# Optimization experiments

Measured on AMD Instinct MI355X. Metric: run time of the kernel, lower is better.

Reference implementation:

```python
import jax, jax.numpy as jnp
import numpy as np

B, T, C, H = 2, 2048, 1024, 16
D = C // H  # head dim = 64

def setup_inputs() -> dict:
    key = jax.random.key(0)
    k1, k2, k3 = jax.random.split(key, 3)
    x = jax.random.normal(k1, (B, T, C), dtype=jnp.float32)
    Wqkv = jax.random.normal(k2, (C, 3 * C), dtype=jnp.float32) * (1.0 / np.sqrt(C))
    bqkv = jnp.zeros((3 * C,), dtype=jnp.float32)
    Wo = jax.random.normal(k3, (C, C), dtype=jnp.float32) * (1.0 / np.sqrt(C))
    bo = jnp.zeros((C,), dtype=jnp.float32)
    return {"x": x, "Wqkv": Wqkv, "bqkv": bqkv, "Wo": Wo, "bo": bo}

def reference(x, Wqkv, bqkv, Wo, bo):
    b, t, c = x.shape
    qkv = x @ Wqkv + bqkv                              # [B,T,3C]
    q, k, v = jnp.split(qkv, 3, axis=-1)
    # [B,T,C] -> [B,H,T,D]
    q = q.reshape(b, t, H, D).transpose(0, 2, 1, 3)
    k = k.reshape(b, t, H, D).transpose(0, 2, 1, 3)
    v = v.reshape(b, t, H, D).transpose(0, 2, 1, 3)
    scores = jnp.einsum('bhqd,bhkd->bhqk', q, k) * (1.0 / np.sqrt(D))
    causal = jnp.tril(jnp.ones((t, t), dtype=bool))
    scores = jnp.where(causal, scores, -jnp.inf)
    probs = jax.nn.softmax(scores, axis=-1)           # dropout p=0 -> identity
    out = jnp.einsum('bhqk,bhkd->bhqd', probs, v)
    out = out.transpose(0, 2, 1, 3).reshape(b, t, c)
    return out @ Wo + bo
```

## Files before the change

kernel.cpp:

```cpp
#include <hip/hip_runtime.h>
#include <hip/hip_bf16.h>

typedef __attribute__((ext_vector_type(8))) short bf16x8;
typedef __attribute__((ext_vector_type(4))) short bf16x4;
typedef __attribute__((ext_vector_type(4))) float f32x4;

static __device__ __forceinline__ __hip_bfloat16 f2b(float f) {
    return __float2bfloat16(f);
}
static __device__ __forceinline__ unsigned pack2(float a, float b) {
    unsigned ua = (unsigned)__bfloat16_as_ushort(__float2bfloat16(a));
    unsigned ub = (unsigned)__bfloat16_as_ushort(__float2bfloat16(b));
    return ua | (ub << 16);
}
static __device__ __forceinline__ float exp2fast(float x) {
    return __builtin_amdgcn_exp2f(x);
}

#define QSCALE 0.1803368801111f

__global__ __launch_bounds__(256) void k_prep(
    const float* __restrict__ x, __hip_bfloat16* __restrict__ xb,
    const float* __restrict__ Wqkv, __hip_bfloat16* __restrict__ WqkvT,
    const float* __restrict__ Wo, __hip_bfloat16* __restrict__ WoT)
{
    const int bx = blockIdx.x;
    if (bx < 2048) {
        int i = bx * 256 + threadIdx.x;
        const int stride = 2048 * 256;
        for (; i < 1048576; i += stride) {
            float4 v = reinterpret_cast<const float4*>(x)[i];
            __hip_bfloat16* o = xb + 4 * (size_t)i;
            o[0] = f2b(v.x); o[1] = f2b(v.y); o[2] = f2b(v.z); o[3] = f2b(v.w);
        }
        return;
    }
    __shared__ float tile[32][33];
    const float* in;
    __hip_bfloat16* outp;
    int R, Cn, c0, r0;
    if (bx < 5120) {
        const int b = bx - 2048;
        in = Wqkv; outp = WqkvT; R = 1024; Cn = 3072;
        c0 = (b % 96) * 32; r0 = (b / 96) * 32;
    } else {
        const int b = bx - 5120;
        in = Wo; outp = WoT; R = 1024; Cn = 1024;
        c0 = (b & 31) * 32; r0 = (b >> 5) * 32;
    }
    const int tx = threadIdx.x & 31, ty = threadIdx.x >> 5;
#pragma unroll
    for (int i = 0; i < 32; i += 8)
        tile[ty + i][tx] = in[(size_t)(r0 + ty + i) * Cn + c0 + tx];
    __syncthreads();
#pragma unroll
    for (int i = 0; i < 32; i += 8)
        outp[(size_t)(c0 + ty + i) * R + r0 + tx] = f2b(tile[tx][ty + i]);
}

#define QK_STAGE(buf, kt)                                                       \
    {                                                                           \
        const int k0_ = (kt) << 5;                                              \
        _Pragma("unroll")                                                       \
        for (int i = 0; i < 2; ++i) {                                           \
            const int idx = i * 256 + tid;                                      \
            const int r_ = idx >> 2;                                            \
            const int j_ = idx & 3;                                             \
            const int js_ = j_ ^ ((r_ >> 1) & 3);                               \
            __builtin_amdgcn_global_load_lds(                                   \
                (const __attribute__((address_space(1))) void*)(A + (size_t)(m0 + r_) * K + k0_ + js_ * 8), \
                (__attribute__((address_space(3))) void*)(&As[buf][r_][j_ * 8]), 16, 0, 0); \
        }                                                                       \
        _Pragma("unroll")                                                       \
        for (int i = 0; i < 2; ++i) {                                           \
            const int idx = i * 256 + tid;                                      \
            const int r_ = idx >> 2;                                            \
            const int j_ = idx & 3;                                             \
            const int js_ = j_ ^ ((r_ >> 1) & 3);                               \
            __builtin_amdgcn_global_load_lds(                                   \
                (const __attribute__((address_space(1))) void*)(Bt + (size_t)(n0 + r_) * K + k0_ + js_ * 8), \
                (__attribute__((address_space(3))) void*)(&Bs[buf][r_][j_ * 8]), 16, 0, 0); \
        }                                                                       \
    }

__global__ __launch_bounds__(256, 3) void k_gemm_qkv(
    const __hip_bfloat16* __restrict__ A,
    const __hip_bfloat16* __restrict__ Bt,
    const float* __restrict__ bias,
    int K,
    __hip_bfloat16* __restrict__ Qb,
    __hip_bfloat16* __restrict__ Kb,
    __hip_bfloat16* __restrict__ Vt)
{
    __shared__ __hip_bfloat16 As[3][128][32];
    __shared__ __hip_bfloat16 Bs[3][128][32];

    const int tid = threadIdx.x;
    const int lane = tid & 63;
    const int wid = tid >> 6;
    const int wm = wid >> 1, wn = wid & 1;
    const int m0 = blockIdx.y * 128, n0 = blockIdx.x * 128;
    const int l15 = lane & 15, lg = lane >> 4;
    const int rchunk = (lg ^ ((l15 >> 1) & 3)) * 8;

    f32x4 acc[4][4] = {};
    const int nt = K >> 5;

    QK_STAGE(0, 0);
    QK_STAGE(1, 1);
    asm volatile("s_waitcnt vmcnt(4)" ::: "memory");
    __builtin_amdgcn_sched_barrier(0);
    __builtin_amdgcn_s_barrier();
    __builtin_amdgcn_sched_barrier(0);

    for (int t = 0; t < nt; ++t) {
        const int cur = t % 3;
        if (t + 2 < nt) {
            const int nxt = (t + 2) % 3;
            QK_STAGE(nxt, t + 2);
        }
        bf16x8 a[4], bb[4];
#pragma unroll
        for (int m = 0; m < 4; ++m)
            a[m] = *(const bf16x8*)&As[cur][wm * 64 + m * 16 + l15][rchunk];
#pragma unroll
        for (int n = 0; n < 4; ++n)
            bb[n] = *(const bf16x8*)&Bs[cur][wn * 64 + n * 16 + l15][rchunk];
        __builtin_amdgcn_s_setprio(1);
#pragma unroll
        for (int m = 0; m < 4; ++m)
#pragma unroll
            for (int n = 0; n < 4; ++n)
                acc[m][n] = __builtin_amdgcn_mfma_f32_16x16x32_bf16(a[m], bb[n], acc[m][n], 0, 0, 0);
        __builtin_amdgcn_s_setprio(0);
        __builtin_amdgcn_sched_barrier(0);
        if (t + 2 < nt)
            asm volatile("s_waitcnt vmcnt(4)" ::: "memory");
        else
            asm volatile("s_waitcnt vmcnt(0)" ::: "memory");
        __builtin_amdgcn_sched_barrier(0);
        __builtin_amdgcn_s_barrier();
        __builtin_amdgcn_sched_barrier(0);
    }

#pragma unroll
    for (int m = 0; m < 4; ++m) {
        const int row = m0 + wm * 64 + m * 16 + lg * 4;
#pragma unroll
        for (int n = 0; n < 4; ++n) {
            const int col = n0 + wn * 64 + n * 16 + l15;
            const float bv = bias[col];
#pragma unroll
            for (int r = 0; r < 4; ++r) {
                const float val = acc[m][n][r] + bv;
                const int rr = row + r;
                const int sec = col >> 10, cw = col & 1023;
                const int hh = cw >> 6, d = cw & 63;
                const int bq = rr >> 11, tt = rr & 2047;
                const int bh = bq * 16 + hh;
                if (sec == 0)
                    Qb[((size_t)bh * 2048 + tt) * 64 + d] = f2b(val * QSCALE);
                else if (sec == 1)
                    Kb[((size_t)bh * 2048 + tt) * 64 + d] = f2b(val);
                else
                    Vt[((size_t)bh * 64 + d) * 2048 + tt] = f2b(val);
            }
        }
    }
}

#define OUT_STAGE(buf, kt)                                                      \
    {                                                                           \
        const int k0_ = (kt) << 5;                                              \
        _Pragma("unroll")                                                       \
        for (int i = 0; i < 2; ++i) {                                           \
            const int idx = i * 256 + tid;                                      \
            const int r_ = idx >> 2;                                            \
            const int j_ = idx & 3;                                             \
            const int js_ = j_ ^ ((r_ >> 1) & 3);                               \
            __builtin_amdgcn_global_load_lds(                                   \
                (const __attribute__((address_space(1))) void*)(A + (size_t)(m0 + r_) * K + k0_ + js_ * 8), \
                (__attribute__((address_space(3))) void*)(&As[buf][r_][j_ * 8]), 16, 0, 0); \
        }                                                                       \
        {                                                                       \
            const int r_ = tid >> 2;                                            \
            const int j_ = tid & 3;                                             \
            const int js_ = j_ ^ ((r_ >> 1) & 3);                               \
            __builtin_amdgcn_global_load_lds(                                   \
                (const __attribute__((address_space(1))) void*)(Bt + (size_t)(n0 + r_) * K + k0_ + js_ * 8), \
                (__attribute__((address_space(3))) void*)(&Bs[buf][r_][j_ * 8]), 16, 0, 0); \
        }                                                                       \
    }

__global__ __launch_bounds__(256, 4) void k_gemm_out(
    const __hip_bfloat16* __restrict__ A,
    const __hip_bfloat16* __restrict__ Bt,
    const float* __restrict__ bias,
    int K, int Nn,
    float* __restrict__ outf)
{
    __shared__ __hip_bfloat16 As[3][128][32];
    __shared__ __hip_bfloat16 Bs[3][64][32];

    const int tid = threadIdx.x;
    const int lane = tid & 63;
    const int wid = tid >> 6;
    const int wm = wid >> 1, wn = wid & 1;
    const int m0 = blockIdx.y * 128, n0 = blockIdx.x * 64;
    const int l15 = lane & 15, lg = lane >> 4;
    const int rchunk = (lg ^ ((l15 >> 1) & 3)) * 8;

    f32x4 acc[4][2] = {};
    const int nt = K >> 5;

    OUT_STAGE(0, 0);
    OUT_STAGE(1, 1);
    asm volatile("s_waitcnt vmcnt(3)" ::: "memory");
    __builtin_amdgcn_sched_barrier(0);
    __builtin_amdgcn_s_barrier();
    __builtin_amdgcn_sched_barrier(0);

    for (int t = 0; t < nt; ++t) {
        const int cur = t % 3;
        if (t + 2 < nt) {
            const int nxt = (t + 2) % 3;
            OUT_STAGE(nxt, t + 2);
        }
        bf16x8 a[4], bb[2];
#pragma unroll
        for (int m = 0; m < 4; ++m)
            a[m] = *(const bf16x8*)&As[cur][wm * 64 + m * 16 + l15][rchunk];
#pragma unroll
        for (int n = 0; n < 2; ++n)
            bb[n] = *(const bf16x8*)&Bs[cur][wn * 32 + n * 16 + l15][rchunk];
        __builtin_amdgcn_s_setprio(1);
#pragma unroll
        for (int m = 0; m < 4; ++m)
#pragma unroll
            for (int n = 0; n < 2; ++n)
                acc[m][n] = __builtin_amdgcn_mfma_f32_16x16x32_bf16(a[m], bb[n], acc[m][n], 0, 0, 0);
        __builtin_amdgcn_s_setprio(0);
        __builtin_amdgcn_sched_barrier(0);
        if (t + 2 < nt)
            asm volatile("s_waitcnt vmcnt(3)" ::: "memory");
        else
            asm volatile("s_waitcnt vmcnt(0)" ::: "memory");
        __builtin_amdgcn_sched_barrier(0);
        __builtin_amdgcn_s_barrier();
        __builtin_amdgcn_sched_barrier(0);
    }

#pragma unroll
    for (int m = 0; m < 4; ++m) {
        const int row = m0 + wm * 64 + m * 16 + lg * 4;
#pragma unroll
        for (int n = 0; n < 2; ++n) {
            const int col = n0 + wn * 32 + n * 16 + l15;
            const float bv = bias[col];
#pragma unroll
            for (int r = 0; r < 4; ++r)
                outf[(size_t)(row + r) * Nn + col] = acc[m][n][r] + bv;
        }
    }
}

#define DEFER_THR 4.0f

#define AT_STAGE(buf, tt)                                                       \
    {                                                                           \
        const int ks_ = (tt) << 6;                                              \
        _Pragma("unroll")                                                       \
        for (int i = 0; i < 2; ++i) {                                           \
            const int idx = i * 256 + tid;                                      \
            const int r_ = idx >> 3;                                            \
            const int j_ = idx & 7;                                             \
            const int js_ = j_ ^ (r_ & 7);                                      \
            __builtin_amdgcn_global_load_lds(                                   \
                (const __attribute__((address_space(1))) void*)(Kbase + (size_t)(ks_ + r_) * 64 + js_ * 8), \
                (__attribute__((address_space(3))) void*)(&Ks[buf][r_][j_ * 8]), 16, 0, 0); \
        }                                                                       \
        _Pragma("unroll")                                                       \
        for (int i = 0; i < 2; ++i) {                                           \
            const int idx = i * 256 + tid;                                      \
            const int r_ = idx >> 3;                                            \
            const int j_ = idx & 7;                                             \
            const int js_ = j_ ^ (r_ & 7);                                      \
            __builtin_amdgcn_global_load_lds(                                   \
                (const __attribute__((address_space(1))) void*)(Vbase + (size_t)r_ * 2048 + ks_ + js_ * 8), \
                (__attribute__((address_space(3))) void*)(&Vs[buf][r_][j_ * 8]), 16, 0, 0); \
        }                                                                       \
    }

#define FULL_STEP_L(BUF)                                                        \
    {                                                                           \
        bf16x8 bk0[4], bk1[4];                                                  \
        _Pragma("unroll")                                                       \
        for (int kf = 0; kf < 4; ++kf) {                                        \
            bk0[kf] = *(const bf16x8*)&Ks[BUF][kf * 16 + l15][(lg ^ kswz) * 8]; \
            bk1[kf] = *(const bf16x8*)&Ks[BUF][kf * 16 + l15][((4 + lg) ^ kswz) * 8]; \
        }                                                                       \
        f32x4 s0[4] = {}, s1[4] = {};                                           \
        __builtin_amdgcn_s_setprio(1);                                          \
        _Pragma("unroll")                                                       \
        for (int kf = 0; kf < 4; ++kf) {                                        \
            s0[kf] = __builtin_amdgcn_mfma_f32_16x16x32_bf16(bk0[kf], aq[0][0], s0[kf], 0, 0, 0); \
            s0[kf] = __builtin_amdgcn_mfma_f32_16x16x32_bf16(bk1[kf], aq[0][1], s0[kf], 0, 0, 0); \
            s1[kf] = __builtin_amdgcn_mfma_f32_16x16x32_bf16(bk0[kf], aq[1][0], s1[kf], 0, 0, 0); \
            s1[kf] = __builtin_amdgcn_mfma_f32_16x16x32_bf16(bk1[kf], aq[1][1], s1[kf], 0, 0, 0); \
        }                                                                       \
        __builtin_amdgcn_s_setprio(0);                                          \
        float px0 = fmaxf(fmaxf(fmaxf(s0[0][0], s0[0][1]), fmaxf(s0[0][2], s0[0][3])), \
                          fmaxf(fmaxf(s0[1][0], s0[1][1]), fmaxf(s0[1][2], s0[1][3]))); \
        px0 = fmaxf(px0, fmaxf(fmaxf(fmaxf(s0[2][0], s0[2][1]), fmaxf(s0[2][2], s0[2][3])), \
                               fmaxf(fmaxf(s0[3][0], s0[3][1]), fmaxf(s0[3][2], s0[3][3])))); \
        float px1 = fmaxf(fmaxf(fmaxf(s1[0][0], s1[0][1]), fmaxf(s1[0][2], s1[0][3])), \
                          fmaxf(fmaxf(s1[1][0], s1[1][1]), fmaxf(s1[1][2], s1[1][3]))); \
        px1 = fmaxf(px1, fmaxf(fmaxf(fmaxf(s1[2][0], s1[2][1]), fmaxf(s1[2][2], s1[2][3])), \
                               fmaxf(fmaxf(s1[3][0], s1[3][1]), fmaxf(s1[3][2], s1[3][3])))); \
        px0 = fmaxf(px0, __shfl_xor(px0, 16));                                  \
        px0 = fmaxf(px0, __shfl_xor(px0, 32));                                  \
        px1 = fmaxf(px1, __shfl_xor(px1, 16));                                  \
        px1 = fmaxf(px1, __shfl_xor(px1, 32));                                  \
        if (__any((px0 > m0 + DEFER_THR) || (px1 > m1 + DEFER_THR))) {          \
            const float mn0 = fmaxf(m0, px0), mn1 = fmaxf(m1, px1);             \
            const float al0 = exp2fast(m0 - mn0), al1 = exp2fast(m1 - mn1);     \
            m0 = mn0; m1 = mn1;                                                 \
            l0 *= al0; l1 *= al1;                                               \
            _Pragma("unroll")                                                   \
            for (int dc = 0; dc < 4; ++dc)                                      \
                _Pragma("unroll")                                               \
                for (int r = 0; r < 4; ++r) {                                   \
                    o[0][dc][r] *= al0;                                         \
                    o[1][dc][r] *= al1;                                         \
                }                                                               \
        }                                                                       \
        float rs0 = 0.f, rs1 = 0.f;                                             \
        _Pragma("unroll")                                                       \
        for (int kf = 0; kf < 4; ++kf) {                                        \
            _Pragma("unroll")                                                   \
            for (int r = 0; r < 4; ++r) {                                       \
                s0[kf][r] = exp2fast(s0[kf][r] - m0);                           \
                s1[kf][r] = exp2fast(s1[kf][r] - m1);                           \
                rs0 += s0[kf][r];                                               \
                rs1 += s1[kf][r];                                               \
            }                                                                   \
            uint2 w0, w1;                                                       \
            w0.x = pack2(s0[kf][0], s0[kf][1]); w0.y = pack2(s0[kf][2], s0[kf][3]); \
            w1.x = pack2(s1[kf][0], s1[kf][1]); w1.y = pack2(s1[kf][2], s1[kf][3]); \
            const int off = l15 * 64 + ((kf * 16 + lg * 4) ^ swz);              \
            *(uint2*)&Pw0[off] = w0;                                            \
            *(uint2*)&Pw1[off] = w1;                                            \
        }                                                                       \
        rs0 += __shfl_xor(rs0, 16); rs0 += __shfl_xor(rs0, 32);                 \
        rs1 += __shfl_xor(rs1, 16); rs1 += __shfl_xor(rs1, 32);                 \
        l0 += rs0; l1 += rs1;                                                   \
        _Pragma("unroll")                                                       \
        for (int c2 = 0; c2 < 2; ++c2) {                                        \
            bf16x8 bv[4];                                                       \
            _Pragma("unroll")                                                   \
            for (int dc = 0; dc < 4; ++dc)                                      \
                bv[dc] = *(const bf16x8*)&Vs[BUF][dc * 16 + l15][(((c2 << 2) | lg) ^ kswz) * 8]; \
            const int off = l15 * 64 + ((c2 * 32 + lg * 8) ^ swz);              \
            const bf16x8 pb0 = *(const bf16x8*)&Pw0[off];                       \
            const bf16x8 pb1 = *(const bf16x8*)&Pw1[off];                       \
            __builtin_amdgcn_s_setprio(1);                                      \
            _Pragma("unroll")                                                   \
            for (int dc = 0; dc < 4; ++dc) {                                    \
                o[0][dc] = __builtin_amdgcn_mfma_f32_16x16x32_bf16(bv[dc], pb0, o[0][dc], 0, 0, 0); \
                o[1][dc] = __builtin_amdgcn_mfma_f32_16x16x32_bf16(bv[dc], pb1, o[1][dc], 0, 0, 0); \
            }                                                                   \
            __builtin_amdgcn_s_setprio(0);                                      \
        }                                                                       \
    }

#define TAIL_STEP_L(BUF)                                                        \
    {                                                                           \
        const int ks_ = nfull * 64;                                             \
        float mr[2] = {m0, m1}, lr[2] = {l0, l1};                               \
        _Pragma("unroll")                                                       \
        for (int qf = 0; qf < 2; ++qf) {                                        \
            const int qlo = qw + qf * 16;                                       \
            const int qv = qlo + l15;                                           \
            bf16x8 bk0[4], bk1[4];                                              \
            _Pragma("unroll")                                                   \
            for (int kf = 0; kf < 4; ++kf) {                                    \
                bk0[kf] = *(const bf16x8*)&Ks[BUF][kf * 16 + l15][(lg ^ kswz) * 8]; \
                bk1[kf] = *(const bf16x8*)&Ks[BUF][kf * 16 + l15][((4 + lg) ^ kswz) * 8]; \
            }                                                                   \
            f32x4 s[4] = {};                                                    \
            _Pragma("unroll")                                                   \
            for (int kf = 0; kf < 4; ++kf) {                                    \
                if (ks_ + kf * 16 <= qlo + 15) {                                \
                    s[kf] = __builtin_amdgcn_mfma_f32_16x16x32_bf16(bk0[kf], aq[qf][0], s[kf], 0, 0, 0); \
                    s[kf] = __builtin_amdgcn_mfma_f32_16x16x32_bf16(bk1[kf], aq[qf][1], s[kf], 0, 0, 0); \
                }                                                               \
            }                                                                   \
            const int kb = ks_ + lg * 4;                                        \
            _Pragma("unroll")                                                   \
            for (int kf = 0; kf < 4; ++kf)                                      \
                _Pragma("unroll")                                               \
                for (int r = 0; r < 4; ++r)                                     \
                    s[kf][r] = (kb + kf * 16 + r <= qv) ? s[kf][r] : -1e30f;    \
            float mx = fmaxf(fmaxf(fmaxf(s[0][0], s[0][1]), fmaxf(s[0][2], s[0][3])), \
                             fmaxf(fmaxf(s[1][0], s[1][1]), fmaxf(s[1][2], s[1][3]))); \
            mx = fmaxf(mx, fmaxf(fmaxf(fmaxf(s[2][0], s[2][1]), fmaxf(s[2][2], s[2][3])), \
                                 fmaxf(fmaxf(s[3][0], s[3][1]), fmaxf(s[3][2], s[3][3])))); \
            mx = fmaxf(mx, __shfl_xor(mx, 16));                                 \
            mx = fmaxf(mx, __shfl_xor(mx, 32));                                 \
            const float mnew = fmaxf(mr[qf], mx);                               \
            const float al = exp2fast(mr[qf] - mnew);                           \
            mr[qf] = mnew;                                                      \
            float rs = 0.f;                                                     \
            _Pragma("unroll")                                                   \
            for (int kf = 0; kf < 4; ++kf)                                      \
                _Pragma("unroll")                                               \
                for (int r = 0; r < 4; ++r) {                                   \
                    s[kf][r] = exp2fast(s[kf][r] - mnew);                       \
                    rs += s[kf][r];                                             \
                }                                                               \
            rs += __shfl_xor(rs, 16);                                           \
            rs += __shfl_xor(rs, 32);                                           \
            lr[qf] = lr[qf] * al + rs;                                          \
            _Pragma("unroll")                                                   \
            for (int dc = 0; dc < 4; ++dc)                                      \
                _Pragma("unroll")                                               \
                for (int r = 0; r < 4; ++r) o[qf][dc][r] *= al;                 \
            __hip_bfloat16* Pw = (qf == 0) ? Pw0 : Pw1;                         \
            _Pragma("unroll")                                                   \
            for (int kf = 0; kf < 4; ++kf) {                                    \
                uint2 w;                                                        \
                w.x = pack2(s[kf][0], s[kf][1]);                                \
                w.y = pack2(s[kf][2], s[kf][3]);                                \
                *(uint2*)&Pw[l15 * 64 + ((kf * 16 + lg * 4) ^ swz)] = w;        \
            }                                                                   \
            _Pragma("unroll")                                                   \
            for (int c2 = 0; c2 < 2; ++c2) {                                    \
                if (ks_ + c2 * 32 <= qlo + 15) {                                \
                    bf16x8 bv[4];                                               \
                    _Pragma("unroll")                                           \
                    for (int dc = 0; dc < 4; ++dc)                              \
                        bv[dc] = *(const bf16x8*)&Vs[BUF][dc * 16 + l15][(((c2 << 2) | lg) ^ kswz) * 8]; \
                    const bf16x8 pb = *(const bf16x8*)&Pw[l15 * 64 + ((c2 * 32 + lg * 8) ^ swz)]; \
                    _Pragma("unroll")                                           \
                    for (int dc = 0; dc < 4; ++dc)                              \
                        o[qf][dc] = __builtin_amdgcn_mfma_f32_16x16x32_bf16(bv[dc], pb, o[qf][dc], 0, 0, 0); \
                }                                                               \
            }                                                                   \
        }                                                                       \
        l0 = lr[0]; l1 = lr[1];                                                 \
    }

__global__ __launch_bounds__(256, 2) void k_attn(
    const __hip_bfloat16* __restrict__ Qb,
    const __hip_bfloat16* __restrict__ Kb,
    const __hip_bfloat16* __restrict__ Vt,
    __hip_bfloat16* __restrict__ att)
{
    __shared__ __hip_bfloat16 Ks[3][64][64];
    __shared__ __hip_bfloat16 Vs[3][64][64];
    __shared__ __hip_bfloat16 P_lds[4][2][16 * 64];
    const int tid = threadIdx.x, lane = tid & 63, wid = tid >> 6;
    const int lid = blockIdx.x;
    const int xcd = lid & 7, j = lid >> 3;
    const int jj = j >> 2;
    const int tile = (jj < 8) ? (15 - jj) : (jj - 8);
    const int bh = xcd * 4 + (j & 3);
    const int q0 = tile * 128;
    const int qw = q0 + wid * 32;
    const int l15 = lane & 15, lg = lane >> 4;
    const int swz = (l15 & 7) << 3;
    const int kswz = l15 & 7;

    const __hip_bfloat16* Qbase = Qb + (size_t)bh * 2048 * 64;
    const __hip_bfloat16* Kbase = Kb + (size_t)bh * 2048 * 64;
    const __hip_bfloat16* Vbase = Vt + (size_t)bh * 64 * 2048;

    bf16x8 aq[2][2];
#pragma unroll
    for (int qf = 0; qf < 2; ++qf)
#pragma unroll
        for (int c = 0; c < 2; ++c)
            aq[qf][c] = *(const bf16x8*)(Qbase + (size_t)(qw + qf * 16 + l15) * 64 + c * 32 + lg * 8);

    f32x4 o[2][4] = {};
    float m0 = -1e30f, m1 = -1e30f, l0 = 0.f, l1 = 0.f;

    const int nfull = qw >> 6;
    const int NT = 2 * tile + 2;
    __hip_bfloat16* Pw0 = &P_lds[wid][0][0];
    __hip_bfloat16* Pw1 = &P_lds[wid][1][0];

    AT_STAGE(0, 0);
    AT_STAGE(1, 1);
    asm volatile("s_waitcnt vmcnt(4)" ::: "memory");
    __builtin_amdgcn_sched_barrier(0);
    __builtin_amdgcn_s_barrier();
    __builtin_amdgcn_sched_barrier(0);

    for (int tt = 0; tt < NT; ++tt) {
        const int cur = tt % 3;
        if (tt + 2 < NT) {
            const int nxt = (tt + 2) % 3;
            AT_STAGE(nxt, tt + 2);
        }
        if (tt < nfull) {
            FULL_STEP_L(cur);
        } else if (tt == nfull) {
            TAIL_STEP_L(cur);
        }
        __builtin_amdgcn_sched_barrier(0);
        if (tt + 2 < NT)
            asm volatile("s_waitcnt vmcnt(4)" ::: "memory");
        else
            asm volatile("s_waitcnt vmcnt(0)" ::: "memory");
        __builtin_amdgcn_sched_barrier(0);
        __builtin_amdgcn_s_barrier();
        __builtin_amdgcn_sched_barrier(0);
    }

    const int bq = bh >> 4, hh = bh & 15;
    const float inv0 = 1.0f / l0, inv1 = 1.0f / l1;
#pragma unroll
    for (int qf = 0; qf < 2; ++qf) {
        const float inv = (qf == 0) ? inv0 : inv1;
        const size_t rowb = ((size_t)(bq * 2048 + qw + qf * 16 + l15)) * 1024 + hh * 64;
#pragma unroll
        for (int dc = 0; dc < 4; ++dc) {
            bf16x4 st;
#pragma unroll
            for (int r = 0; r < 4; ++r)
                st[r] = (short)__bfloat16_as_ushort(__float2bfloat16(o[qf][dc][r] * inv));
            *(bf16x4*)(att + rowb + dc * 16 + lg * 4) = st;
        }
    }
}

extern "C" void kernel_launch(void* const* d_in, const int* in_sizes, int n_in,
                              void* d_out, int out_size, void* d_ws, size_t ws_size,
                              hipStream_t stream)
{
    const float* x    = (const float*)d_in[0];
    const float* Wqkv = (const float*)d_in[1];
    const float* bqkv = (const float*)d_in[2];
    const float* Wo   = (const float*)d_in[3];
    const float* bo   = (const float*)d_in[4];
    float* out = (float*)d_out;

    char* ws = (char*)d_ws;
    const size_t MB = 1024 * 1024;
    __hip_bfloat16* xb    = (__hip_bfloat16*)(ws);
    __hip_bfloat16* WqkvT = (__hip_bfloat16*)(ws + 8 * MB);
    __hip_bfloat16* WoT   = (__hip_bfloat16*)(ws + 14 * MB);
    __hip_bfloat16* Qb    = (__hip_bfloat16*)(ws + 16 * MB);
    __hip_bfloat16* Kb    = (__hip_bfloat16*)(ws + 24 * MB);
    __hip_bfloat16* Vt    = (__hip_bfloat16*)(ws + 32 * MB);
    __hip_bfloat16* att   = (__hip_bfloat16*)(ws + 40 * MB);

    k_prep<<<6144, 256, 0, stream>>>(x, xb, Wqkv, WqkvT, Wo, WoT);

    k_gemm_qkv<<<dim3(24, 32), 256, 0, stream>>>(
        xb, WqkvT, bqkv, 1024, Qb, Kb, Vt);

    k_attn<<<512, 256, 0, stream>>>(Qb, Kb, Vt, att);

    k_gemm_out<<<dim3(16, 32), 256, 0, stream>>>(
        att, WoT, bo, 1024, 1024, out);
}
```

Measured before the change: 128.6 us.

## Software-pipeline QK^T of the next tile with softmax and PV of the current one

Splits each attention step into a QK^T MFMA phase and a softmax/PV phase, then ping-pongs two score register sets so the next tile's QK^T MFMAs are issued alongside the current tile's exponentials and PV MFMAs. The main loop is unrolled by two to alternate the register sets. The causal tail is restructured to reuse the precomputed unmasked scores, so its per-fragment MFMA skipping is dropped. The per-step wait now drains all outstanding global-to-LDS loads (vmcnt(0)), and the last steps issue redundant clamped loads. This adds register pressure and shortens prefetch slack in exchange for better MFMA/VALU overlap.

```diff
diff --git a/kernel.cpp b/kernel.cpp
--- a/kernel.cpp
+++ b/kernel.cpp
@@ -291,32 +291,38 @@
         }                                                                       \
     }
 
-#define FULL_STEP_L(BUF)                                                        \
-    {                                                                           \
+#define QK_COMP(SN0, SN1, TI)                                                   \
+    {                                                                           \
+        const int kb_ = (TI) % 3;                                               \
         bf16x8 bk0[4], bk1[4];                                                  \
         _Pragma("unroll")                                                       \
         for (int kf = 0; kf < 4; ++kf) {                                        \
-            bk0[kf] = *(const bf16x8*)&Ks[BUF][kf * 16 + l15][(lg ^ kswz) * 8]; \
-            bk1[kf] = *(const bf16x8*)&Ks[BUF][kf * 16 + l15][((4 + lg) ^ kswz) * 8]; \
-        }                                                                       \
-        f32x4 s0[4] = {}, s1[4] = {};                                           \
+            bk0[kf] = *(const bf16x8*)&Ks[kb_][kf * 16 + l15][(lg ^ kswz) * 8]; \
+            bk1[kf] = *(const bf16x8*)&Ks[kb_][kf * 16 + l15][((4 + lg) ^ kswz) * 8]; \
+        }                                                                       \
         __builtin_amdgcn_s_setprio(1);                                          \
         _Pragma("unroll")                                                       \
         for (int kf = 0; kf < 4; ++kf) {                                        \
-            s0[kf] = __builtin_amdgcn_mfma_f32_16x16x32_bf16(bk0[kf], aq[0][0], s0[kf], 0, 0, 0); \
-            s0[kf] = __builtin_amdgcn_mfma_f32_16x16x32_bf16(bk1[kf], aq[0][1], s0[kf], 0, 0, 0); \
-            s1[kf] = __builtin_amdgcn_mfma_f32_16x16x32_bf16(bk0[kf], aq[1][0], s1[kf], 0, 0, 0); \
-            s1[kf] = __builtin_amdgcn_mfma_f32_16x16x32_bf16(bk1[kf], aq[1][1], s1[kf], 0, 0, 0); \
+            f32x4 z_ = {};                                                      \
+            SN0[kf] = __builtin_amdgcn_mfma_f32_16x16x32_bf16(bk0[kf], aq[0][0], z_, 0, 0, 0); \
+            SN0[kf] = __builtin_amdgcn_mfma_f32_16x16x32_bf16(bk1[kf], aq[0][1], SN0[kf], 0, 0, 0); \
+            SN1[kf] = __builtin_amdgcn_mfma_f32_16x16x32_bf16(bk0[kf], aq[1][0], z_, 0, 0, 0); \
+            SN1[kf] = __builtin_amdgcn_mfma_f32_16x16x32_bf16(bk1[kf], aq[1][1], SN1[kf], 0, 0, 0); \
         }                                                                       \
         __builtin_amdgcn_s_setprio(0);                                          \
-        float px0 = fmaxf(fmaxf(fmaxf(s0[0][0], s0[0][1]), fmaxf(s0[0][2], s0[0][3])), \
-                          fmaxf(fmaxf(s0[1][0], s0[1][1]), fmaxf(s0[1][2], s0[1][3]))); \
-        px0 = fmaxf(px0, fmaxf(fmaxf(fmaxf(s0[2][0], s0[2][1]), fmaxf(s0[2][2], s0[2][3])), \
-                               fmaxf(fmaxf(s0[3][0], s0[3][1]), fmaxf(s0[3][2], s0[3][3])))); \
-        float px1 = fmaxf(fmaxf(fmaxf(s1[0][0], s1[0][1]), fmaxf(s1[0][2], s1[0][3])), \
-                          fmaxf(fmaxf(s1[1][0], s1[1][1]), fmaxf(s1[1][2], s1[1][3]))); \
-        px1 = fmaxf(px1, fmaxf(fmaxf(fmaxf(s1[2][0], s1[2][1]), fmaxf(s1[2][2], s1[2][3])), \
-                               fmaxf(fmaxf(s1[3][0], s1[3][1]), fmaxf(s1[3][2], s1[3][3])))); \
+    }
+
+#define PROC_FULL(SC0, SC1, TI)                                                 \
+    {                                                                           \
+        const int vb_ = (TI) % 3;                                               \
+        float px0 = fmaxf(fmaxf(fmaxf(SC0[0][0], SC0[0][1]), fmaxf(SC0[0][2], SC0[0][3])), \
+                          fmaxf(fmaxf(SC0[1][0], SC0[1][1]), fmaxf(SC0[1][2], SC0[1][3]))); \
+        px0 = fmaxf(px0, fmaxf(fmaxf(fmaxf(SC0[2][0], SC0[2][1]), fmaxf(SC0[2][2], SC0[2][3])), \
+                               fmaxf(fmaxf(SC0[3][0], SC0[3][1]), fmaxf(SC0[3][2], SC0[3][3])))); \
+        float px1 = fmaxf(fmaxf(fmaxf(SC1[0][0], SC1[0][1]), fmaxf(SC1[0][2], SC1[0][3])), \
+                          fmaxf(fmaxf(SC1[1][0], SC1[1][1]), fmaxf(SC1[1][2], SC1[1][3]))); \
+        px1 = fmaxf(px1, fmaxf(fmaxf(fmaxf(SC1[2][0], SC1[2][1]), fmaxf(SC1[2][2], SC1[2][3])), \
+                               fmaxf(fmaxf(SC1[3][0], SC1[3][1]), fmaxf(SC1[3][2], SC1[3][3])))); \
         px0 = fmaxf(px0, __shfl_xor(px0, 16));                                  \
         px0 = fmaxf(px0, __shfl_xor(px0, 32));                                  \
         px1 = fmaxf(px1, __shfl_xor(px1, 16));                                  \
@@ -339,14 +345,14 @@
         for (int kf = 0; kf < 4; ++kf) {                                        \
             _Pragma("unroll")                                                   \
             for (int r = 0; r < 4; ++r) {                                       \
-                s0[kf][r] = exp2fast(s0[kf][r] - m0);                           \
-                s1[kf][r] = exp2fast(s1[kf][r] - m1);                           \
-                rs0 += s0[kf][r];                                               \
-                rs1 += s1[kf][r];                                               \
+                SC0[kf][r] = exp2fast(SC0[kf][r] - m0);                         \
+                SC1[kf][r] = exp2fast(SC1[kf][r] - m1);                         \
+                rs0 += SC0[kf][r];                                              \
+                rs1 += SC1[kf][r];                                              \
             }                                                                   \
             uint2 w0, w1;                                                       \
-            w0.x = pack2(s0[kf][0], s0[kf][1]); w0.y = pack2(s0[kf][2], s0[kf][3]); \
-            w1.x = pack2(s1[kf][0], s1[kf][1]); w1.y = pack2(s1[kf][2], s1[kf][3]); \
+            w0.x = pack2(SC0[kf][0], SC0[kf][1]); w0.y = pack2(SC0[kf][2], SC0[kf][3]); \
+            w1.x = pack2(SC1[kf][0], SC1[kf][1]); w1.y = pack2(SC1[kf][2], SC1[kf][3]); \
             const int off = l15 * 64 + ((kf * 16 + lg * 4) ^ swz);              \
             *(uint2*)&Pw0[off] = w0;                                            \
             *(uint2*)&Pw1[off] = w1;                                            \
@@ -359,7 +365,7 @@
             bf16x8 bv[4];                                                       \
             _Pragma("unroll")                                                   \
             for (int dc = 0; dc < 4; ++dc)                                      \
-                bv[dc] = *(const bf16x8*)&Vs[BUF][dc * 16 + l15][(((c2 << 2) | lg) ^ kswz) * 8]; \
+                bv[dc] = *(const bf16x8*)&Vs[vb_][dc * 16 + l15][(((c2 << 2) | lg) ^ kswz) * 8]; \
             const int off = l15 * 64 + ((c2 * 32 + lg * 8) ^ swz);              \
             const bf16x8 pb0 = *(const bf16x8*)&Pw0[off];                       \
             const bf16x8 pb1 = *(const bf16x8*)&Pw1[off];                       \
@@ -373,81 +379,86 @@
         }                                                                       \
     }
 
-#define TAIL_STEP_L(BUF)                                                        \
-    {                                                                           \
-        const int ks_ = nfull * 64;                                             \
-        float mr[2] = {m0, m1}, lr[2] = {l0, l1};                               \
-        _Pragma("unroll")                                                       \
-        for (int qf = 0; qf < 2; ++qf) {                                        \
-            const int qlo = qw + qf * 16;                                       \
-            const int qv = qlo + l15;                                           \
-            bf16x8 bk0[4], bk1[4];                                              \
-            _Pragma("unroll")                                                   \
-            for (int kf = 0; kf < 4; ++kf) {                                    \
-                bk0[kf] = *(const bf16x8*)&Ks[BUF][kf * 16 + l15][(lg ^ kswz) * 8]; \
-                bk1[kf] = *(const bf16x8*)&Ks[BUF][kf * 16 + l15][((4 + lg) ^ kswz) * 8]; \
+#define PROC_TAIL_QF(SCX, MV, LV, QF, PWX, VB, KS)                              \
+    {                                                                           \
+        const int qlo = qw + (QF) * 16;                                         \
+        const int qv = qlo + l15;                                               \
+        const int kb = (KS) + lg * 4;                                           \
+        _Pragma("unroll")                                                       \
+        for (int kf = 0; kf < 4; ++kf)                                          \
+            _Pragma("unroll")                                                   \
+            for (int r = 0; r < 4; ++r)                                         \
+                SCX[kf][r] = (kb + kf * 16 + r <= qv) ? SCX[kf][r] : -1e30f;    \
+        float mx = fmaxf(fmaxf(fmaxf(SCX[0][0], SCX[0][1]), fmaxf(SCX[0][2], SCX[0][3])), \
+                         fmaxf(fmaxf(SCX[1][0], SCX[1][1]), fmaxf(SCX[1][2], SCX[1][3]))); \
+        mx = fmaxf(mx, fmaxf(fmaxf(fmaxf(SCX[2][0], SCX[2][1]), fmaxf(SCX[2][2], SCX[2][3])), \
+                             fmaxf(fmaxf(SCX[3][0], SCX[3][1]), fmaxf(SCX[3][2], SCX[3][3])))); \
+        mx = fmaxf(mx, __shfl_xor(mx, 16));                                     \
+        mx = fmaxf(mx, __shfl_xor(mx, 32));                                     \
+        const float mnew = fmaxf(MV, mx);                                       \
+        const float al = exp2fast(MV - mnew);                                   \
+        MV = mnew;                                                              \
+        float rs = 0.f;                                                         \
+        _Pragma("unroll")                                                       \
+        for (int kf = 0; kf < 4; ++kf)                                          \
+            _Pragma("unroll")                                                   \
+            for (int r = 0; r < 4; ++r) {                                       \
+                SCX[kf][r] = exp2fast(SCX[kf][r] - mnew);                       \
+                rs += SCX[kf][r];                                               \
             }                                                                   \
-            f32x4 s[4] = {};                                                    \
-            _Pragma("unroll")                                                   \
-            for (int kf = 0; kf < 4; ++kf) {                                    \
-                if (ks_ + kf * 16 <= qlo + 15) {                                \
-                    s[kf] = __builtin_amdgcn_mfma_f32_16x16x32_bf16(bk0[kf], aq[qf][0], s[kf], 0, 0, 0); \
-                    s[kf] = __builtin_amdgcn_mfma_f32_16x16x32_bf16(bk1[kf], aq[qf][1], s[kf], 0, 0, 0); \
-                }                                                               \
+        rs += __shfl_xor(rs, 16);                                               \
+        rs += __shfl_xor(rs, 32);                                               \
+        LV = LV * al + rs;                                                      \
+        _Pragma("unroll")                                                       \
+        for (int dc = 0; dc < 4; ++dc)                                          \
+            _Pragma("unroll")                                                   \
+            for (int r = 0; r < 4; ++r) o[QF][dc][r] *= al;                     \
+        _Pragma("unroll")                                                       \
+        for (int kf = 0; kf < 4; ++kf) {                                        \
+            uint2 w;                                                            \
+            w.x = pack2(SCX[kf][0], SCX[kf][1]);                                \
+            w.y = pack2(SCX[kf][2], SCX[kf][3]);                                \
+            *(uint2*)&PWX[l15 * 64 + ((kf * 16 + lg * 4) ^ swz)] = w;           \
+        }                                                                       \
+        _Pragma("unroll")                                                       \
+        for (int c2 = 0; c2 < 2; ++c2) {                                        \
+            if ((KS) + c2 * 32 <= qlo + 15) {                                   \
+                bf16x8 bv[4];                                                   \
+                _Pragma("unroll")                                               \
+                for (int dc = 0; dc < 4; ++dc)                                  \
+                    bv[dc] = *(const bf16x8*)&Vs[VB][dc * 16 + l15][(((c2 << 2) | lg) ^ kswz) * 8]; \
+                const bf16x8 pb = *(const bf16x8*)&PWX[l15 * 64 + ((c2 * 32 + lg * 8) ^ swz)]; \
+                _Pragma("unroll")                                               \
+                for (int dc = 0; dc < 4; ++dc)                                  \
+                    o[QF][dc] = __builtin_amdgcn_mfma_f32_16x16x32_bf16(bv[dc], pb, o[QF][dc], 0, 0, 0); \
             }                                                                   \
-            const int kb = ks_ + lg * 4;                                        \
-            _Pragma("unroll")                                                   \
-            for (int kf = 0; kf < 4; ++kf)                                      \
-                _Pragma("unroll")                                               \
-                for (int r = 0; r < 4; ++r)                                     \
-                    s[kf][r] = (kb + kf * 16 + r <= qv) ? s[kf][r] : -1e30f;    \
-            float mx = fmaxf(fmaxf(fmaxf(s[0][0], s[0][1]), fmaxf(s[0][2], s[0][3])), \
-                             fmaxf(fmaxf(s[1][0], s[1][1]), fmaxf(s[1][2], s[1][3]))); \
-            mx = fmaxf(mx, fmaxf(fmaxf(fmaxf(s[2][0], s[2][1]), fmaxf(s[2][2], s[2][3])), \
-                                 fmaxf(fmaxf(s[3][0], s[3][1]), fmaxf(s[3][2], s[3][3])))); \
-            mx = fmaxf(mx, __shfl_xor(mx, 16));                                 \
-            mx = fmaxf(mx, __shfl_xor(mx, 32));                                 \
-            const float mnew = fmaxf(mr[qf], mx);                               \
-            const float al = exp2fast(mr[qf] - mnew);                           \
-            mr[qf] = mnew;                                                      \
-            float rs = 0.f;                                                     \
-            _Pragma("unroll")                                                   \
-            for (int kf = 0; kf < 4; ++kf)                                      \
-                _Pragma("unroll")                                               \
-                for (int r = 0; r < 4; ++r) {                                   \
-                    s[kf][r] = exp2fast(s[kf][r] - mnew);                       \
-                    rs += s[kf][r];                                             \
-                }                                                               \
-            rs += __shfl_xor(rs, 16);                                           \
-            rs += __shfl_xor(rs, 32);                                           \
-            lr[qf] = lr[qf] * al + rs;                                          \
-            _Pragma("unroll")                                                   \
-            for (int dc = 0; dc < 4; ++dc)                                      \
-                _Pragma("unroll")                                               \
-                for (int r = 0; r < 4; ++r) o[qf][dc][r] *= al;                 \
-            __hip_bfloat16* Pw = (qf == 0) ? Pw0 : Pw1;                         \
-            _Pragma("unroll")                                                   \
-            for (int kf = 0; kf < 4; ++kf) {                                    \
-                uint2 w;                                                        \
-                w.x = pack2(s[kf][0], s[kf][1]);                                \
-                w.y = pack2(s[kf][2], s[kf][3]);                                \
-                *(uint2*)&Pw[l15 * 64 + ((kf * 16 + lg * 4) ^ swz)] = w;        \
-            }                                                                   \
-            _Pragma("unroll")                                                   \
-            for (int c2 = 0; c2 < 2; ++c2) {                                    \
-                if (ks_ + c2 * 32 <= qlo + 15) {                                \
-                    bf16x8 bv[4];                                               \
-                    _Pragma("unroll")                                           \
-                    for (int dc = 0; dc < 4; ++dc)                              \
-                        bv[dc] = *(const bf16x8*)&Vs[BUF][dc * 16 + l15][(((c2 << 2) | lg) ^ kswz) * 8]; \
-                    const bf16x8 pb = *(const bf16x8*)&Pw[l15 * 64 + ((c2 * 32 + lg * 8) ^ swz)]; \
-                    _Pragma("unroll")                                           \
-                    for (int dc = 0; dc < 4; ++dc)                              \
-                        o[qf][dc] = __builtin_amdgcn_mfma_f32_16x16x32_bf16(bv[dc], pb, o[qf][dc], 0, 0, 0); \
-                }                                                               \
-            }                                                                   \
-        }                                                                       \
-        l0 = lr[0]; l1 = lr[1];                                                 \
+        }                                                                       \
+    }
+
+#define PROC_TAIL(SC0, SC1, TI)                                                 \
+    {                                                                           \
+        const int vb_ = (TI) % 3;                                               \
+        const int kst_ = nfull * 64;                                            \
+        PROC_TAIL_QF(SC0, m0, l0, 0, Pw0, vb_, kst_);                           \
+        PROC_TAIL_QF(SC1, m1, l1, 1, Pw1, vb_, kst_);                           \
+    }
+
+#define PIPE_STEP(SC0, SC1, SN0, SN1, T)                                        \
+    {                                                                           \
+        const int t_ = (T);                                                     \
+        const int ts_ = (t_ + 2 < NT) ? (t_ + 2) : (NT - 1);                    \
+        AT_STAGE((t_ + 2) % 3, ts_);                                            \
+        if (t_ + 1 < NT) QK_COMP(SN0, SN1, t_ + 1);                             \
+        if (t_ < nfull) {                                                       \
+            PROC_FULL(SC0, SC1, t_);                                            \
+        } else if (t_ == nfull) {                                               \
+            PROC_TAIL(SC0, SC1, t_);                                            \
+        }                                                                       \
+        __builtin_amdgcn_sched_barrier(0);                                      \
+        asm volatile("s_waitcnt vmcnt(0)" ::: "memory");                        \
+        __builtin_amdgcn_sched_barrier(0);                                      \
+        __builtin_amdgcn_s_barrier();                                           \
+        __builtin_amdgcn_sched_barrier(0);                                      \
     }
 
 __global__ __launch_bounds__(256, 2) void k_attn(
@@ -490,32 +501,19 @@
     __hip_bfloat16* Pw0 = &P_lds[wid][0][0];
     __hip_bfloat16* Pw1 = &P_lds[wid][1][0];
 
+    f32x4 sA0[4], sA1[4], sB0[4], sB1[4];
+
     AT_STAGE(0, 0);
     AT_STAGE(1, 1);
-    asm volatile("s_waitcnt vmcnt(4)" ::: "memory");
+    asm volatile("s_waitcnt vmcnt(0)" ::: "memory");
     __builtin_amdgcn_sched_barrier(0);
     __builtin_amdgcn_s_barrier();
     __builtin_amdgcn_sched_barrier(0);
-
-    for (int tt = 0; tt < NT; ++tt) {
-        const int cur = tt % 3;
-        if (tt + 2 < NT) {
-            const int nxt = (tt + 2) % 3;
-            AT_STAGE(nxt, tt + 2);
-        }
-        if (tt < nfull) {
-            FULL_STEP_L(cur);
-        } else if (tt == nfull) {
-            TAIL_STEP_L(cur);
-        }
-        __builtin_amdgcn_sched_barrier(0);
-        if (tt + 2 < NT)
-            asm volatile("s_waitcnt vmcnt(4)" ::: "memory");
-        else
-            asm volatile("s_waitcnt vmcnt(0)" ::: "memory");
-        __builtin_amdgcn_sched_barrier(0);
-        __builtin_amdgcn_s_barrier();
-        __builtin_amdgcn_sched_barrier(0);
+    QK_COMP(sA0, sA1, 0);
+
+    for (int tt = 0; tt < NT; tt += 2) {
+        PIPE_STEP(sA0, sA1, sB0, sB1, tt);
+        PIPE_STEP(sB0, sB1, sA0, sA1, tt + 1);
     }
 
     const int bq = bh >> 4, hh = bh & 15;
```

Measured after the change: 129.9 us. About the same (+1.0%).
